# Kernel tuning notes

Hardware: AMD Instinct MI355X
Metric: run time of the kernel (lower is better)

Reference implementation:

```python
import jax, jax.numpy as jnp
import numpy as np

L_LAYERS = 6
DIM = 256
HEADS = 8
FFN = 1024
EPS_LN = 1e-3  # keras LayerNormalization default epsilon
EPS_ATT = 1e-6


def sine_pos_encoding(seq_len, d):
    pos = jnp.arange(seq_len, dtype=jnp.float32)[:, None]
    i = jnp.arange(d, dtype=jnp.float32)[None, :]
    rate = jnp.power(1e4, -(2.0 * jnp.floor(i / 2.0)) / d)
    ang = pos * rate
    return jnp.where(jnp.arange(d)[None, :] % 2 == 0, jnp.sin(ang), jnp.cos(ang))


def layer_norm(x, g, b):
    mu = jnp.mean(x, axis=-1, keepdims=True)
    var = jnp.mean(jnp.square(x - mu), axis=-1, keepdims=True)
    return (x - mu) * jax.lax.rsqrt(var + EPS_LN) * g + b


def lin_attn(xq, xk, xv, Wq, bq, Wk, bk, Wv, bv, Wo, bo):
    B, Lq, _ = xq.shape
    Lk = xk.shape[1]
    dh = DIM // HEADS
    q = (xq @ Wq + bq).reshape(B, Lq, HEADS, dh)
    k = (xk @ Wk + bk).reshape(B, Lk, HEADS, dh)
    v = (xv @ Wv + bv).reshape(B, Lk, HEADS, dh)
    # kernel feature map: elu(x) + 1
    Qf = jax.nn.elu(q) + 1.0
    Kf = jax.nn.elu(k) + 1.0
    KV = jnp.einsum('bshd,bshm->bhdm', Kf, v)            # [B,H,dh,dh]
    Z = 1.0 / (jnp.einsum('blhd,bhd->blh', Qf, Kf.sum(1)) + EPS_ATT)
    out = jnp.einsum('blhd,bhdm,blh->blhm', Qf, KV, Z)   # [B,Lq,H,dh]
    return out.reshape(B, Lq, DIM) @ Wo + bo


def setup_inputs() -> dict:
    key = jax.random.key(0)
    ks = jax.random.split(key, 32)
    s = 0.02
    d = {
        'Q': jax.random.normal(ks[0], (8, 4096, 256), jnp.float32),
        'K': jax.random.normal(ks[1], (8, 4096, 256), jnp.float32),
    }
    def W(k, shape):
        return jax.random.normal(k, shape, jnp.float32) * s
    for sfx, base in (('1', 2), ('2', 10)):
        d['Wq' + sfx] = W(ks[base + 0], (L_LAYERS, DIM, DIM))
        d['Wk' + sfx] = W(ks[base + 1], (L_LAYERS, DIM, DIM))
        d['Wv' + sfx] = W(ks[base + 2], (L_LAYERS, DIM, DIM))
        d['Wo' + sfx] = W(ks[base + 3], (L_LAYERS, DIM, DIM))
        d['bq' + sfx] = jnp.zeros((L_LAYERS, DIM))
        d['bk' + sfx] = jnp.zeros((L_LAYERS, DIM))
        d['bv' + sfx] = jnp.zeros((L_LAYERS, DIM))
        d['bo' + sfx] = jnp.zeros((L_LAYERS, DIM))
    d['Wf1'] = W(ks[20], (L_LAYERS, DIM, FFN))
    d['bf1'] = jnp.zeros((L_LAYERS, FFN))
    d['Wf2'] = W(ks[21], (L_LAYERS, FFN, DIM))
    d['bf2'] = jnp.zeros((L_LAYERS, DIM))
    for nm in ('ln1', 'ln2', 'ln3'):
        d[nm + '_g'] = jnp.ones((L_LAYERS, DIM))
        d[nm + '_b'] = jnp.zeros((L_LAYERS, DIM))
    return d


def reference(Q, K,
              Wq1, Wk1, Wv1, Wo1, bq1, bk1, bv1, bo1,
              Wq2, Wk2, Wv2, Wo2, bq2, bk2, bv2, bo2,
              Wf1, bf1, Wf2, bf2,
              ln1_g, ln1_b, ln2_g, ln2_b, ln3_g, ln3_b):
    pe = sine_pos_encoding(Q.shape[1], Q.shape[2])
    x1 = Q + pe[None]
    for i in range(L_LAYERS):
        x = lin_attn(x1, x1, x1, Wq1[i], bq1[i], Wk1[i], bk1[i], Wv1[i], bv1[i], Wo1[i], bo1[i])
        x2 = layer_norm(x + x1, ln1_g[i], ln1_b[i])
        x = lin_attn(x2, K, K, Wq2[i], bq2[i], Wk2[i], bk2[i], Wv2[i], bv2[i], Wo2[i], bo2[i])
        x3 = layer_norm(x + x2, ln2_g[i], ln2_b[i])
        h = jax.nn.relu(x3 @ Wf1[i] + bf1[i])
        f = jax.nn.relu(h @ Wf2[i] + bf2[i])  # second Dense also has relu
        x1 = layer_norm(f + x3, ln3_g[i], ln3_b[i])
    return x1
```

## Files before the change

kernel.cpp:

```cpp
#include <hip/hip_runtime.h>

#define BATCH 8
#define SEQ 4096
#define DIM 256
#define NH 8
#define DH 32
#define FFN_DIM 1024
#define NL 6
#define M_TOTAL (BATCH * SEQ)
#define NCHUNK 8

typedef __attribute__((ext_vector_type(8))) short s16x8;
typedef __attribute__((ext_vector_type(4))) short s16x4;
typedef __attribute__((ext_vector_type(4))) float f32x4;

__device__ __forceinline__ float bf2f(short s) {
    union { unsigned u; float f; } x;
    x.u = ((unsigned)(unsigned short)s) << 16;
    return x.f;
}
__device__ __forceinline__ short f2bf(float f) {
    union { float f; unsigned u; } x;
    x.f = f;
    unsigned r = x.u + 0x7fffu + ((x.u >> 16) & 1u);
    return (short)(r >> 16);
}

#define GLDS16(gp, sp) __builtin_amdgcn_global_load_lds( \
    (const __attribute__((address_space(1))) void*)(gp), \
    (__attribute__((address_space(3))) void*)(sp), 16, 0, 0)

__device__ __forceinline__ int xcd_chunk(int bx, int nwg) {
    return (bx & 7) * (nwg >> 3) + (bx >> 3);
}

__global__ void peadd_kernel(const float* __restrict__ Q, short* __restrict__ xb,
                             float* __restrict__ xf, int total)
{
    const float c = 9.210340371976184f / 256.f;
    for (int idx = blockIdx.x * 256 + threadIdx.x; idx < total; idx += gridDim.x * 256) {
        int d = idx & (DIM - 1);
        int l = (idx >> 8) & (SEQ - 1);
        float rate = __expf(-(float)(d & ~1) * c);
        float ang = (float)l * rate;
        float pe = (d & 1) ? cosf(ang) : sinf(ang);
        float v = Q[idx] + pe;
        xb[idx] = f2bf(v);
        xf[idx] = v;
    }
}

__global__ void kconv_kernel(const float* __restrict__ src, short* __restrict__ dst, int total)
{
    for (int idx = blockIdx.x * 256 + threadIdx.x; idx < total; idx += gridDim.x * 256)
        dst[idx] = f2bf(src[idx]);
}

__global__ void wtrans_kernel(const float* __restrict__ W, short* __restrict__ Wt,
                              int K, int N, int lstride, int rowoff)
{
    __shared__ float tile[32][33];
    int k0 = blockIdx.x * 32, n0 = blockIdx.y * 32;
    const float* Wl = W + (long)blockIdx.z * K * N;
    short* Wtl = Wt + (long)blockIdx.z * lstride;
    int tx = threadIdx.x, ty = threadIdx.y;
#pragma unroll
    for (int r = 0; r < 4; ++r)
        tile[ty + r * 8][tx] = Wl[(long)(k0 + ty + r * 8) * N + n0 + tx];
    __syncthreads();
#pragma unroll
    for (int r = 0; r < 4; ++r)
        Wtl[(long)(rowoff + n0 + ty + r * 8) * K + k0 + tx] = f2bf(tile[tx][ty + r * 8]);
}

__global__ void bpack_kernel(const float* __restrict__ bk1, const float* __restrict__ bv1,
                             const float* __restrict__ bk2, const float* __restrict__ bv2,
                             float* __restrict__ o1, float* __restrict__ o2)
{
    int z = blockIdx.x, t = threadIdx.x;
    o1[z * 512 + t] = (t < 256) ? bk1[z * 256 + t] : bv1[z * 256 + t - 256];
    o2[z * 512 + t] = (t < 256) ? bk2[z * 256 + t] : bv2[z * 256 + t - 256];
}

template<int ACT>
__global__ __launch_bounds__(256, 2) void gemm_bt_kernel(
    const short* __restrict__ A, const short* __restrict__ Bt,
    const float* __restrict__ bias, short* __restrict__ Cb,
    int N, int K, int lda, int ldc, int eluCut)
{
    __shared__ short As[2][128][64];
    __shared__ short Bs[2][128][64];
    const int tid = threadIdx.x;
    const int lane = tid & 63;
    const int wid = tid >> 6;
    const int wr = wid >> 1, wc = wid & 1;
    const int bx = xcd_chunk(blockIdx.x, gridDim.x);
    const int bm = bx * 128, bn = blockIdx.y * 128;
    const int l15 = lane & 15, l4 = lane >> 4;
    const int rl = lane >> 3;
    const int ch = lane & 7;
    const int nt = K >> 6;

    auto STAGE = [&](int buf, int t) {
        const int k0 = t << 6;
#pragma unroll
        for (int j = 0; j < 8; ++j) {
            int s = wid * 8 + j;
            if (s < 16) {
                int r = s * 8 + rl;
                int cs = ch ^ (r & 7);
                GLDS16(A + (long)(bm + r) * lda + k0 + cs * 8, &As[buf][s * 8][0]);
            } else {
                int r = (s - 16) * 8 + rl;
                int cs = ch ^ (r & 7);
                GLDS16(Bt + (long)(bn + r) * K + k0 + cs * 8, &Bs[buf][(s - 16) * 8][0]);
            }
        }
    };

    f32x4 acc[4][4] = {};

    STAGE(0, 0);
    STAGE(1, 1);
    for (int t = 0; t < nt; ++t) {
        const int buf = t & 1;
        if (t + 1 < nt) { asm volatile("s_waitcnt vmcnt(8)" ::: "memory"); }
        else            { asm volatile("s_waitcnt vmcnt(0)" ::: "memory"); }
        asm volatile("s_barrier" ::: "memory");
        s16x8 avA[2][4], avB[2][4];
        const int sw = l15 & 7;
#pragma unroll
        for (int kk = 0; kk < 2; ++kk) {
#pragma unroll
            for (int m = 0; m < 4; ++m)
                avA[kk][m] = *(const s16x8*)&As[buf][wr * 64 + m * 16 + l15][(((kk << 2) | l4) ^ sw) << 3];
#pragma unroll
            for (int n = 0; n < 4; ++n)
                avB[kk][n] = *(const s16x8*)&Bs[buf][wc * 64 + n * 16 + l15][(((kk << 2) | l4) ^ sw) << 3];
        }
        asm volatile("s_waitcnt lgkmcnt(0)" ::: "memory");
        asm volatile("s_barrier" ::: "memory");
        if (t + 2 < nt) STAGE(buf, t + 2);
#pragma unroll
        for (int kk = 0; kk < 2; ++kk)
#pragma unroll
            for (int m = 0; m < 4; ++m)
#pragma unroll
                for (int n = 0; n < 4; ++n)
                    acc[m][n] = __builtin_amdgcn_mfma_f32_16x16x32_bf16(avA[kk][m], avB[kk][n], acc[m][n], 0, 0, 0);
    }

#pragma unroll
    for (int m = 0; m < 4; ++m) {
        int row0 = bm + wr * 64 + m * 16 + l4 * 4;
#pragma unroll
        for (int n = 0; n < 4; ++n) {
            int col = bn + wc * 64 + n * 16 + l15;
            float bv = bias[col];
#pragma unroll
            for (int j = 0; j < 4; ++j) {
                float v = acc[m][n][j] + bv;
                if (ACT == 1) { if (col < eluCut) v = (v > 0.f) ? v + 1.f : __expf(v); }
                else if (ACT == 2) v = fmaxf(v, 0.f);
                Cb[(long)(row0 + j) * ldc + col] = f2bf(v);
            }
        }
    }
}

__global__ __launch_bounds__(512, 1) void ffnln_kernel(
    const short* __restrict__ X, const short* __restrict__ W1t,
    const float* __restrict__ b1, const short* __restrict__ W2t,
    const float* __restrict__ b2,
    const float* __restrict__ gam, const float* __restrict__ bet,
    const float* __restrict__ Fin, float* __restrict__ Fout,
    short* __restrict__ xb)
{
    __shared__ short xs[4][64][64];
    __shared__ short hs[4][64][64];
    __shared__ short Bs[8][2][32][64];
    __shared__ float partS[8][64];
    __shared__ float partQ[8][64];
    __shared__ float muA[64];
    __shared__ float rsA[64];
    const int tid = threadIdx.x;
    const int lane = tid & 63;
    const int w = tid >> 6;
    const int bm = xcd_chunk(blockIdx.x, gridDim.x) * 64;
    const int l15 = lane & 15, l4 = lane >> 4;
    const int rl = lane >> 3;
    const int ch = lane & 7;
    const int sw = l15 & 7;

#pragma unroll
    for (int j = 0; j < 4; ++j) {
        int s = w * 4 + j;
        int kt = s >> 3, rg = s & 7;
        int r = rg * 8 + rl;
        int cs = ch ^ (r & 7);
        GLDS16(X + (long)(bm + r) * 256 + kt * 64 + cs * 8, &xs[kt][rg * 8][0]);
    }
    auto STAGEB = [&](int buf, int v) {
        int hc = v >> 3, u = v & 7;
#pragma unroll
        for (int j = 0; j < 4; ++j) {
            int lr = j * 8 + rl;
            int r = w * 32 + lr;
            int cs = ch ^ (lr & 7);
            const short* src = (u < 4)
                ? W1t + (long)(hc * 256 + r) * 256 + u * 64 + cs * 8
                : W2t + (long)r * 1024 + hc * 256 + (u - 4) * 64 + cs * 8;
            GLDS16(src, &Bs[w][buf][j * 8][0]);
        }
    };

    STAGEB(0, 0);
    STAGEB(1, 1);
    asm volatile("s_waitcnt vmcnt(8)" ::: "memory");
    asm volatile("s_barrier" ::: "memory");

    f32x4 facc[4][2] = {};

    for (int hc = 0; hc < 4; ++hc) {
        f32x4 hacc[4][2] = {};
#pragma unroll
        for (int u = 0; u < 4; ++u) {
            const int v = hc * 8 + u;
            const int buf = v & 1;
            asm volatile("s_waitcnt vmcnt(4)" ::: "memory");
            s16x8 avA[2][4], avB[2][2];
#pragma unroll
            for (int kk = 0; kk < 2; ++kk) {
#pragma unroll
                for (int n = 0; n < 2; ++n)
                    avB[kk][n] = *(const s16x8*)&Bs[w][buf][n * 16 + l15][(((kk << 2) | l4) ^ sw) << 3];
#pragma unroll
                for (int m = 0; m < 4; ++m)
                    avA[kk][m] = *(const s16x8*)&xs[u][m * 16 + l15][(((kk << 2) | l4) ^ sw) << 3];
            }
            asm volatile("s_waitcnt lgkmcnt(0)" ::: "memory");
            STAGEB(buf, v + 2);
#pragma unroll
            for (int kk = 0; kk < 2; ++kk)
#pragma unroll
                for (int m = 0; m < 4; ++m)
#pragma unroll
                    for (int n = 0; n < 2; ++n)
                        hacc[m][n] = __builtin_amdgcn_mfma_f32_16x16x32_bf16(avA[kk][m], avB[kk][n], hacc[m][n], 0, 0, 0);
        }
        asm volatile("s_waitcnt lgkmcnt(0)" ::: "memory");
        asm volatile("s_barrier" ::: "memory");
#pragma unroll
        for (int m = 0; m < 4; ++m)
#pragma unroll
            for (int n = 0; n < 2; ++n) {
                int c = w * 32 + n * 16 + l15;
                float bv = b1[hc * 256 + c];
#pragma unroll
                for (int j = 0; j < 4; ++j) {
                    int r = m * 16 + l4 * 4 + j;
                    float hv = fmaxf(hacc[m][n][j] + bv, 0.f);
                    int kt = c >> 6, cc = (c & 63) >> 3;
                    hs[kt][r][((cc ^ (r & 7)) << 3) + (c & 7)] = f2bf(hv);
                }
            }
        asm volatile("s_waitcnt lgkmcnt(0)" ::: "memory");
        asm volatile("s_barrier" ::: "memory");
#pragma unroll
        for (int u = 4; u < 8; ++u) {
            const int v = hc * 8 + u;
            const int buf = v & 1;
            if (v < 31) { asm volatile("s_waitcnt vmcnt(4)" ::: "memory"); }
            else        { asm volatile("s_waitcnt vmcnt(0)" ::: "memory"); }
            s16x8 avA[2][4], avB[2][2];
#pragma unroll
            for (int kk = 0; kk < 2; ++kk) {
#pragma unroll
                for (int n = 0; n < 2; ++n)
                    avB[kk][n] = *(const s16x8*)&Bs[w][buf][n * 16 + l15][(((kk << 2) | l4) ^ sw) << 3];
#pragma unroll
                for (int m = 0; m < 4; ++m)
                    avA[kk][m] = *(const s16x8*)&hs[u - 4][m * 16 + l15][(((kk << 2) | l4) ^ sw) << 3];
            }
            asm volatile("s_waitcnt lgkmcnt(0)" ::: "memory");
            if (v + 2 < 32) STAGEB(buf, v + 2);
#pragma unroll
            for (int kk = 0; kk < 2; ++kk)
#pragma unroll
                for (int m = 0; m < 4; ++m)
#pragma unroll
                    for (int n = 0; n < 2; ++n)
                        facc[m][n] = __builtin_amdgcn_mfma_f32_16x16x32_bf16(avA[kk][m], avB[kk][n], facc[m][n], 0, 0, 0);
        }
    }

#pragma unroll
    for (int m = 0; m < 4; ++m)
#pragma unroll
        for (int n = 0; n < 2; ++n) {
            int col = w * 32 + n * 16 + l15;
            float bv = b2[col];
#pragma unroll
            for (int j = 0; j < 4; ++j) {
                int r = m * 16 + l4 * 4 + j;
                float v = fmaxf(facc[m][n][j] + bv, 0.f);
                v += Fin[(long)(bm + r) * DIM + col];
                facc[m][n][j] = v;
            }
        }
#pragma unroll
    for (int m = 0; m < 4; ++m)
#pragma unroll
        for (int j = 0; j < 4; ++j) {
            float s = facc[m][0][j] + facc[m][1][j];
            float q = facc[m][0][j] * facc[m][0][j] + facc[m][1][j] * facc[m][1][j];
#pragma unroll
            for (int off = 1; off < 16; off <<= 1) {
                s += __shfl_xor(s, off);
                q += __shfl_xor(q, off);
            }
            if (l15 == 0) {
                partS[w][m * 16 + l4 * 4 + j] = s;
                partQ[w][m * 16 + l4 * 4 + j] = q;
            }
        }
    __syncthreads();
    if (tid < 64) {
        float S = 0, Qq = 0;
#pragma unroll
        for (int ww = 0; ww < 8; ++ww) { S += partS[ww][tid]; Qq += partQ[ww][tid]; }
        float mu = S * (1.f / 256.f);
        float var = Qq * (1.f / 256.f) - mu * mu;
        muA[tid] = mu;
        rsA[tid] = rsqrtf(var + 1e-3f);
    }
    __syncthreads();
#pragma unroll
    for (int m = 0; m < 4; ++m)
#pragma unroll
        for (int j = 0; j < 4; ++j) {
            int r = m * 16 + l4 * 4 + j;
            float mu = muA[r], rs = rsA[r];
#pragma unroll
            for (int n = 0; n < 2; ++n) {
                int col = w * 32 + n * 16 + l15;
                float t = (facc[m][n][j] - mu) * rs * gam[col] + bet[col];
                long o = (long)(bm + r) * DIM + col;
                xb[o] = f2bf(t);
                Fout[o] = t;
            }
        }
}

__global__ __launch_bounds__(512, 1) void qattn_kernel(
    const short* __restrict__ A, const short* __restrict__ Bt,
    const float* __restrict__ bias, const float* __restrict__ kv,
    const float* __restrict__ ksum,
    const short* __restrict__ WoT, const float* __restrict__ bo,
    const float* __restrict__ gam, const float* __restrict__ bet,
    const float* __restrict__ Fin, float* __restrict__ Fout,
    short* __restrict__ xb)
{
    __shared__ char smem[140288];
    short (*As)[128][64] = (short(*)[128][64])(smem);
    short (*Bs)[256][64] = (short(*)[256][64])(smem + 32768);
    short (*QfL)[256] = (short(*)[256])(smem);
    short (*kvbT)[32][48] = (short(*)[32][48])(smem + 98304);
    float* ksumAll = (float*)(smem + 122880);
    float (*partDenH)[128] = (float(*)[128])(smem + 123904);
    short (*oL)[256] = (short(*)[256])(smem + 65536);
    short (*WoS)[256][64] = (short(*)[256][64])(smem);
    float (*partS)[128] = (float(*)[128])(smem + 131072);
    float (*partQ)[128] = (float(*)[128])(smem + 135168);
    float* muA = (float*)(smem + 139264);
    float* rsA = (float*)(smem + 139776);

    const int tid = threadIdx.x;
    const int lane = tid & 63;
    const int w = tid >> 6;
    const int wr = w >> 2, wc = w & 3;
    const int bm = xcd_chunk(blockIdx.x, gridDim.x) * 128;
    const int b = bm >> 12;
    const int l15 = lane & 15, l4 = lane >> 4;
    const int rl = lane >> 3;
    const int ch = lane & 7;
    const int sw = l15 & 7;

    for (int idx = tid; idx < 8192; idx += 512) {
        int h = idx >> 10, j = idx & 1023, d = j >> 5, m = j & 31;
        kvbT[h][m][d] = f2bf(kv[(long)(b * 8 + h) * 1024 + j]);
    }
    if (tid < 256) ksumAll[tid] = ksum[(b * 8 + (tid >> 5)) * 32 + (tid & 31)];

    auto STAGE = [&](int buf, int t) {
        const int k0 = t << 6;
#pragma unroll
        for (int j = 0; j < 6; ++j) {
            int s = w * 6 + j;
            if (s < 16) {
                int r = s * 8 + rl;
                int cs = ch ^ (r & 7);
                GLDS16(A + (long)(bm + r) * 256 + k0 + cs * 8, &As[buf][s * 8][0]);
            } else {
                int r = (s - 16) * 8 + rl;
                int cs = ch ^ (r & 7);
                GLDS16(Bt + (long)r * 256 + k0 + cs * 8, &Bs[buf][(s - 16) * 8][0]);
            }
        }
    };

    f32x4 acc[4][4] = {};

    STAGE(0, 0);
    STAGE(1, 1);
#pragma unroll
    for (int t = 0; t < 4; ++t) {
        const int buf = t & 1;
        if (t < 3) { asm volatile("s_waitcnt vmcnt(6)" ::: "memory"); }
        else       { asm volatile("s_waitcnt vmcnt(0)" ::: "memory"); }
        asm volatile("s_barrier" ::: "memory");
        s16x8 avA[2][4], avB[2][4];
#pragma unroll
        for (int kk = 0; kk < 2; ++kk) {
#pragma unroll
            for (int m = 0; m < 4; ++m)
                avA[kk][m] = *(const s16x8*)&As[buf][wr * 64 + m * 16 + l15][(((kk << 2) | l4) ^ sw) << 3];
#pragma unroll
            for (int n = 0; n < 4; ++n)
                avB[kk][n] = *(const s16x8*)&Bs[buf][wc * 64 + n * 16 + l15][(((kk << 2) | l4) ^ sw) << 3];
        }
        asm volatile("s_waitcnt lgkmcnt(0)" ::: "memory");
        asm volatile("s_barrier" ::: "memory");
        if (t < 2) STAGE(buf, t + 2);
#pragma unroll
        for (int kk = 0; kk < 2; ++kk)
#pragma unroll
            for (int m = 0; m < 4; ++m)
#pragma unroll
                for (int n = 0; n < 4; ++n)
                    acc[m][n] = __builtin_amdgcn_mfma_f32_16x16x32_bf16(avA[kk][m], avB[kk][n], acc[m][n], 0, 0, 0);
    }

#pragma unroll
    for (int m = 0; m < 4; ++m)
#pragma unroll
        for (int n = 0; n < 4; ++n) {
            int col = wc * 64 + n * 16 + l15;
            float bv = bias[col];
#pragma unroll
            for (int j = 0; j < 4; ++j) {
                float v = acc[m][n][j] + bv;
                acc[m][n][j] = (v > 0.f) ? v + 1.f : __expf(v);
            }
        }
#pragma unroll
    for (int m = 0; m < 4; ++m)
#pragma unroll
        for (int j = 0; j < 4; ++j) {
            float p0 = acc[m][0][j] * ksumAll[wc * 64 + l15]
                     + acc[m][1][j] * ksumAll[wc * 64 + 16 + l15];
            float p1 = acc[m][2][j] * ksumAll[wc * 64 + 32 + l15]
                     + acc[m][3][j] * ksumAll[wc * 64 + 48 + l15];
#pragma unroll
            for (int off = 1; off < 16; off <<= 1) {
                p0 += __shfl_xor(p0, off);
                p1 += __shfl_xor(p1, off);
            }
            if (l15 == 0) {
                int r = wr * 64 + m * 16 + l4 * 4 + j;
                partDenH[wc * 2 + 0][r] = p0;
                partDenH[wc * 2 + 1][r] = p1;
            }
        }
#pragma unroll
    for (int m = 0; m < 4; ++m)
#pragma unroll
        for (int n = 0; n < 4; ++n) {
            int col = wc * 64 + n * 16 + l15;
#pragma unroll
            for (int j = 0; j < 4; ++j) {
                int r = wr * 64 + m * 16 + l4 * 4 + j;
                int chunk = (col >> 3) ^ (r & 7);
                QfL[r][chunk * 8 + (col & 7)] = f2bf(acc[m][n][j]);
            }
        }
    __syncthreads();

    const int h = w;
    s16x8 afr[2];
#pragma unroll
    for (int ct = 0; ct < 2; ++ct)
        afr[ct] = *(const s16x8*)&kvbT[h][ct * 16 + l15][l4 * 8];
    float zv[8];
#pragma unroll
    for (int rt = 0; rt < 8; ++rt)
        zv[rt] = 1.f / (partDenH[h][rt * 16 + l15] + 1e-6f);
    asm volatile("s_waitcnt lgkmcnt(0)" ::: "memory");
    __syncthreads();

#pragma unroll
    for (int rt = 0; rt < 8; ++rt) {
        int r = rt * 16 + l15;
        int qchunk = (h * 4 + l4) ^ (r & 7);
        s16x8 bfr = *(const s16x8*)&QfL[r][qchunk * 8];
#pragma unroll
        for (int ct = 0; ct < 2; ++ct) {
            f32x4 zero = {0.f, 0.f, 0.f, 0.f};
            f32x4 po = __builtin_amdgcn_mfma_f32_16x16x32_bf16(afr[ct], bfr, zero, 0, 0, 0);
            s16x4 o4;
#pragma unroll
            for (int j = 0; j < 4; ++j) o4[j] = f2bf(po[j] * zv[rt]);
            int c0 = h * 32 + ct * 16 + l4 * 4;
            int cc = c0 >> 3;
            *(s16x4*)&oL[r][((cc ^ (r & 7)) << 3) + (c0 & 7)] = o4;
        }
    }
    asm volatile("s_waitcnt lgkmcnt(0)" ::: "memory");
    __syncthreads();

    auto STAGEWO = [&](int buf, int t) {
#pragma unroll
        for (int j = 0; j < 4; ++j) {
            int lr = j * 8 + rl;
            int r = w * 32 + lr;
            int cs = ch ^ (lr & 7);
            GLDS16(WoT + (long)r * 256 + t * 64 + cs * 8, &WoS[buf][w * 32 + j * 8][0]);
        }
    };
    STAGEWO(0, 0);
    STAGEWO(1, 1);

    f32x4 facc[8][2] = {};
#pragma unroll
    for (int t = 0; t < 4; ++t) {
        const int buf = t & 1;
        if (t < 3) { asm volatile("s_waitcnt vmcnt(4)" ::: "memory"); }
        else       { asm volatile("s_waitcnt vmcnt(0)" ::: "memory"); }
#pragma unroll
        for (int kk = 0; kk < 2; ++kk) {
            s16x8 avB0 = *(const s16x8*)&WoS[buf][w * 32 + l15][(((kk << 2) | l4) ^ sw) << 3];
            s16x8 avB1 = *(const s16x8*)&WoS[buf][w * 32 + 16 + l15][(((kk << 2) | l4) ^ sw) << 3];
#pragma unroll
            for (int m = 0; m < 8; ++m) {
                int ar = m * 16 + l15;
                s16x8 avA = *(const s16x8*)&oL[ar][(t * 8 + (((kk << 2) | l4) ^ sw)) << 3];
                facc[m][0] = __builtin_amdgcn_mfma_f32_16x16x32_bf16(avA, avB0, facc[m][0], 0, 0, 0);
                facc[m][1] = __builtin_amdgcn_mfma_f32_16x16x32_bf16(avA, avB1, facc[m][1], 0, 0, 0);
            }
        }
        asm volatile("s_waitcnt lgkmcnt(0)" ::: "memory");
        if (t + 2 < 4) STAGEWO(buf, t + 2);
    }

#pragma unroll
    for (int m = 0; m < 8; ++m)
#pragma unroll
        for (int n = 0; n < 2; ++n) {
            int col = w * 32 + n * 16 + l15;
            float bv = bo[col];
#pragma unroll
            for (int j = 0; j < 4; ++j) {
                int r = m * 16 + l4 * 4 + j;
                float v = facc[m][n][j] + bv;
                v += Fin[(long)(bm + r) * DIM + col];
                facc[m][n][j] = v;
            }
        }
#pragma unroll
    for (int m = 0; m < 8; ++m)
#pragma unroll
        for (int j = 0; j < 4; ++j) {
            float s = facc[m][0][j] + facc[m][1][j];
            float q = facc[m][0][j] * facc[m][0][j] + facc[m][1][j] * facc[m][1][j];
#pragma unroll
            for (int off = 1; off < 16; off <<= 1) {
                s += __shfl_xor(s, off);
                q += __shfl_xor(q, off);
            }
            if (l15 == 0) {
                partS[w][m * 16 + l4 * 4 + j] = s;
                partQ[w][m * 16 + l4 * 4 + j] = q;
            }
        }
    __syncthreads();
    if (tid < 128) {
        float S = 0, Qq = 0;
#pragma unroll
        for (int ww = 0; ww < 8; ++ww) { S += partS[ww][tid]; Qq += partQ[ww][tid]; }
        float mu = S * (1.f / 256.f);
        float var = Qq * (1.f / 256.f) - mu * mu;
        muA[tid] = mu;
        rsA[tid] = rsqrtf(var + 1e-3f);
    }
    __syncthreads();
#pragma unroll
    for (int m = 0; m < 8; ++m)
#pragma unroll
        for (int j = 0; j < 4; ++j) {
            int r = m * 16 + l4 * 4 + j;
            float mu = muA[r], rs = rsA[r];
#pragma unroll
            for (int n = 0; n < 2; ++n) {
                int col = w * 32 + n * 16 + l15;
                float t = (facc[m][n][j] - mu) * rs * gam[col] + bet[col];
                long o = (long)(bm + r) * DIM + col;
                xb[o] = f2bf(t);
                Fout[o] = t;
            }
        }
}

__global__ __launch_bounds__(256) void kvpart_kernel(
    const short* __restrict__ KV, float* __restrict__ part)
{
    __shared__ float kfs[32][32];
    __shared__ float vsh[32][32];
    int flat = blockIdx.x + (blockIdx.y << 3);
    int b = flat & 7;
    int hh = (flat >> 3) & 7, c = flat >> 6;
    int bh = b * 8 + hh;
    int tid = threadIdx.x;
    int d = tid >> 3, m0 = (tid & 7) * 4;
    float acc0 = 0, acc1 = 0, acc2 = 0, acc3 = 0, ks = 0;
    long rowBase = ((long)b * SEQ + c * 512) * 512 + hh * DH;
    int lrow = (tid & 127) >> 2, cg = tid & 3;
    for (int s0 = 0; s0 < 512; s0 += 32) {
        long rb = rowBase + (long)(s0 + lrow) * 512 + cg * 8 + ((tid < 128) ? 0 : 256);
        s16x8 v8 = *(const s16x8*)(KV + rb);
        float* dst = (tid < 128) ? &kfs[lrow][cg * 8] : &vsh[lrow][cg * 8];
#pragma unroll
        for (int e = 0; e < 8; ++e) dst[e] = bf2f(v8[e]);
        __syncthreads();
#pragma unroll
        for (int s = 0; s < 32; ++s) {
            float kd = kfs[s][d];
            acc0 += kd * vsh[s][m0];
            acc1 += kd * vsh[s][m0 + 1];
            acc2 += kd * vsh[s][m0 + 2];
            acc3 += kd * vsh[s][m0 + 3];
        }
        if (tid < 32) {
#pragma unroll
            for (int s = 0; s < 32; ++s) ks += kfs[s][tid];
        }
        __syncthreads();
    }
    float* pb = part + ((long)bh * NCHUNK + c) * 1056;
    pb[tid * 4 + 0] = acc0; pb[tid * 4 + 1] = acc1;
    pb[tid * 4 + 2] = acc2; pb[tid * 4 + 3] = acc3;
    if (tid < 32) pb[1024 + tid] = ks;
}

__global__ __launch_bounds__(256) void kvred_kernel(
    const float* __restrict__ part, float* __restrict__ kv, float* __restrict__ ksum)
{
    int bh = blockIdx.x, tid = threadIdx.x;
    const float* pb = part + (long)bh * NCHUNK * 1056;
    float s0 = 0, s1 = 0, s2 = 0, s3 = 0;
    for (int cc = 0; cc < NCHUNK; ++cc) {
        const float* p = pb + cc * 1056 + tid * 4;
        s0 += p[0]; s1 += p[1]; s2 += p[2]; s3 += p[3];
    }
    float* kb = kv + (long)bh * 1024 + tid * 4;
    kb[0] = s0; kb[1] = s1; kb[2] = s2; kb[3] = s3;
    if (tid < 32) {
        float ss = 0;
        for (int cc = 0; cc < NCHUNK; ++cc) ss += pb[cc * 1056 + 1024 + tid];
        ksum[bh * 32 + tid] = ss;
    }
}

extern "C" void kernel_launch(void* const* d_in, const int* in_sizes, int n_in,
                              void* d_out, int out_size, void* d_ws, size_t ws_size,
                              hipStream_t stream)
{
    const float* Qin = (const float*)d_in[0];
    const float* Kin = (const float*)d_in[1];
    const float* Wq1 = (const float*)d_in[2];
    const float* Wk1 = (const float*)d_in[3];
    const float* Wv1 = (const float*)d_in[4];
    const float* Wo1 = (const float*)d_in[5];
    const float* bq1 = (const float*)d_in[6];
    const float* bk1 = (const float*)d_in[7];
    const float* bv1 = (const float*)d_in[8];
    const float* bo1 = (const float*)d_in[9];
    const float* Wq2 = (const float*)d_in[10];
    const float* Wk2 = (const float*)d_in[11];
    const float* Wv2 = (const float*)d_in[12];
    const float* Wo2 = (const float*)d_in[13];
    const float* bq2 = (const float*)d_in[14];
    const float* bk2 = (const float*)d_in[15];
    const float* bv2 = (const float*)d_in[16];
    const float* bo2 = (const float*)d_in[17];
    const float* Wf1 = (const float*)d_in[18];
    const float* bf1 = (const float*)d_in[19];
    const float* Wf2 = (const float*)d_in[20];
    const float* bf2 = (const float*)d_in[21];
    const float* ln1g = (const float*)d_in[22];
    const float* ln1b = (const float*)d_in[23];
    const float* ln2g = (const float*)d_in[24];
    const float* ln2b = (const float*)d_in[25];
    const float* ln3g = (const float*)d_in[26];
    const float* ln3b = (const float*)d_in[27];
    (void)in_sizes; (void)n_in; (void)out_size;

    const size_t NEED = 117841920ULL;
    if (ws_size < NEED) return;

    char* ws = (char*)d_ws;
    size_t off = 0;
    auto alloc = [&](size_t bytes) -> void* {
        void* p = ws + off;
        off = (off + bytes + 255) & ~(size_t)255;
        return p;
    };
    const size_t ACT_E = (size_t)M_TOTAL * DIM;

    short* wkv1t = (short*)alloc((size_t)NL * 512 * 256 * 2);
    short* wkv2t = (short*)alloc((size_t)NL * 512 * 256 * 2);
    short* wq1t  = (short*)alloc((size_t)NL * 65536 * 2);
    short* wo1t  = (short*)alloc((size_t)NL * 65536 * 2);
    short* wq2t  = (short*)alloc((size_t)NL * 65536 * 2);
    short* wo2t  = (short*)alloc((size_t)NL * 65536 * 2);
    short* wf1t  = (short*)alloc((size_t)NL * 262144 * 2);
    short* wf2t  = (short*)alloc((size_t)NL * 262144 * 2);
    float* bkv1  = (float*)alloc((size_t)NL * 512 * 4);
    float* bkv2  = (float*)alloc((size_t)NL * 512 * 4);
    short* kbf = (short*)alloc(ACT_E * 2);
    short* A0  = (short*)alloc(ACT_E * 2);
    short* BIG = (short*)alloc((size_t)M_TOTAL * 512 * 2);
    float* Fx  = (float*)alloc(ACT_E * 4);
    float* part = (float*)alloc((size_t)64 * NCHUNK * 1056 * 4);
    float* kvb  = (float*)alloc((size_t)64 * 1024 * 4);
    float* ksb  = (float*)alloc((size_t)64 * 32 * 4);

    peadd_kernel<<<2048, 256, 0, stream>>>(Qin, A0, Fx, (int)ACT_E);
    kconv_kernel<<<2048, 256, 0, stream>>>(Kin, kbf, (int)ACT_E);
    wtrans_kernel<<<dim3(8, 8, NL), dim3(32, 8), 0, stream>>>(Wk1, wkv1t, 256, 256, 512 * 256, 0);
    wtrans_kernel<<<dim3(8, 8, NL), dim3(32, 8), 0, stream>>>(Wv1, wkv1t, 256, 256, 512 * 256, 256);
    wtrans_kernel<<<dim3(8, 8, NL), dim3(32, 8), 0, stream>>>(Wk2, wkv2t, 256, 256, 512 * 256, 0);
    wtrans_kernel<<<dim3(8, 8, NL), dim3(32, 8), 0, stream>>>(Wv2, wkv2t, 256, 256, 512 * 256, 256);
    wtrans_kernel<<<dim3(8, 8, NL), dim3(32, 8), 0, stream>>>(Wq1, wq1t, 256, 256, 65536, 0);
    wtrans_kernel<<<dim3(8, 8, NL), dim3(32, 8), 0, stream>>>(Wo1, wo1t, 256, 256, 65536, 0);
    wtrans_kernel<<<dim3(8, 8, NL), dim3(32, 8), 0, stream>>>(Wq2, wq2t, 256, 256, 65536, 0);
    wtrans_kernel<<<dim3(8, 8, NL), dim3(32, 8), 0, stream>>>(Wo2, wo2t, 256, 256, 65536, 0);
    wtrans_kernel<<<dim3(8, 32, NL), dim3(32, 8), 0, stream>>>(Wf1, wf1t, 256, 1024, 262144, 0);
    wtrans_kernel<<<dim3(32, 8, NL), dim3(32, 8), 0, stream>>>(Wf2, wf2t, 1024, 256, 262144, 0);
    bpack_kernel<<<NL, 512, 0, stream>>>(bk1, bv1, bk2, bv2, bkv1, bkv2);

    dim3 blk(256), blk512(512);

    for (int i = 0; i < NL; ++i) {
        const short* wkv1i = wkv1t + (size_t)i * 512 * 256;
        const short* wkv2i = wkv2t + (size_t)i * 512 * 256;
        const short* wq1i = wq1t + (size_t)i * 65536;
        const short* wo1i = wo1t + (size_t)i * 65536;
        const short* wq2i = wq2t + (size_t)i * 65536;
        const short* wo2i = wo2t + (size_t)i * 65536;
        const short* wf1i = wf1t + (size_t)i * 262144;
        const short* wf2i = wf2t + (size_t)i * 262144;

        gemm_bt_kernel<1><<<dim3(256, 4), blk, 0, stream>>>(A0, wkv1i, bkv1 + i * 512, BIG, 512, 256, 256, 512, 256);
        kvpart_kernel<<<dim3(NCHUNK, 64), blk, 0, stream>>>(BIG, part);
        kvred_kernel<<<64, blk, 0, stream>>>(part, kvb, ksb);
        qattn_kernel<<<M_TOTAL / 128, blk512, 0, stream>>>(A0, wq1i, bq1 + i * 256, kvb, ksb,
            wo1i, bo1 + i * 256, ln1g + i * 256, ln1b + i * 256, Fx, Fx, A0);

        gemm_bt_kernel<1><<<dim3(256, 4), blk, 0, stream>>>(kbf, wkv2i, bkv2 + i * 512, BIG, 512, 256, 256, 512, 256);
        kvpart_kernel<<<dim3(NCHUNK, 64), blk, 0, stream>>>(BIG, part);
        kvred_kernel<<<64, blk, 0, stream>>>(part, kvb, ksb);
        qattn_kernel<<<M_TOTAL / 128, blk512, 0, stream>>>(A0, wq2i, bq2 + i * 256, kvb, ksb,
            wo2i, bo2 + i * 256, ln2g + i * 256, ln2b + i * 256, Fx, Fx, A0);

        ffnln_kernel<<<M_TOTAL / 64, blk512, 0, stream>>>(A0, wf1i, bf1 + i * 1024,
            wf2i, bf2 + i * 256, ln3g + i * 256, ln3b + i * 256,
            Fx, (i == NL - 1) ? (float*)d_out : Fx, A0);
    }
}
```

Before: 1.359 ms.

## Fuse K/V projection with per-chunk KV outer-product reduction using MFMA

The K/V projection GEMM now stages its 128-row, two-head output tile (Kf after elu+1, and V) transposed in shared memory. It then computes the per-chunk Kf^T·V partial and the Kf column sums directly with MFMA, so the bf16 K/V intermediate no longer makes a round trip through global memory. The separate scalar FP32 kvpart kernel and the BIG buffer are removed. In exchange, NCHUNK rises to 32, so kvred sums four times more partials, and the Kf/V values are rounded to bf16 before the MFMA reduction.

Measured after the change: 1.124 ms, median of 2. 1.21x faster.

```diff
diff --git a/kernel.cpp b/kernel.cpp
--- a/kernel.cpp
+++ b/kernel.cpp
@@ -8,7 +8,7 @@
 #define FFN_DIM 1024
 #define NL 6
 #define M_TOTAL (BATCH * SEQ)
-#define NCHUNK 8
+#define NCHUNK 32
 
 typedef __attribute__((ext_vector_type(8))) short s16x8;
 typedef __attribute__((ext_vector_type(4))) short s16x4;
@@ -82,11 +82,9 @@
     o2[z * 512 + t] = (t < 256) ? bk2[z * 256 + t] : bv2[z * 256 + t - 256];
 }
 
-template<int ACT>
-__global__ __launch_bounds__(256, 2) void gemm_bt_kernel(
-    const short* __restrict__ A, const short* __restrict__ Bt,
-    const float* __restrict__ bias, short* __restrict__ Cb,
-    int N, int K, int lda, int ldc, int eluCut)
+__global__ __launch_bounds__(256, 2) void kvproj_kernel(
+    const short* __restrict__ A, const short* __restrict__ WkvT,
+    const float* __restrict__ bkv, float* __restrict__ part)
 {
     __shared__ short As[2][128][64];
     __shared__ short Bs[2][128][64];
@@ -94,12 +92,14 @@
     const int lane = tid & 63;
     const int wid = tid >> 6;
     const int wr = wid >> 1, wc = wid & 1;
+    const int p = blockIdx.y;
     const int bx = xcd_chunk(blockIdx.x, gridDim.x);
-    const int bm = bx * 128, bn = blockIdx.y * 128;
+    const int bm = bx * 128;
+    const int b = bx >> 5, chunk = bx & 31;
     const int l15 = lane & 15, l4 = lane >> 4;
     const int rl = lane >> 3;
     const int ch = lane & 7;
-    const int nt = K >> 6;
+    const int sw = l15 & 7;
 
     auto STAGE = [&](int buf, int t) {
         const int k0 = t << 6;
@@ -109,11 +109,12 @@
             if (s < 16) {
                 int r = s * 8 + rl;
                 int cs = ch ^ (r & 7);
-                GLDS16(A + (long)(bm + r) * lda + k0 + cs * 8, &As[buf][s * 8][0]);
+                GLDS16(A + (long)(bm + r) * 256 + k0 + cs * 8, &As[buf][s * 8][0]);
             } else {
                 int r = (s - 16) * 8 + rl;
+                int srcRow = (r < 64) ? (p * 64 + r) : (256 + p * 64 + (r - 64));
                 int cs = ch ^ (r & 7);
-                GLDS16(Bt + (long)(bn + r) * K + k0 + cs * 8, &Bs[buf][(s - 16) * 8][0]);
+                GLDS16(WkvT + (long)srcRow * 256 + k0 + cs * 8, &Bs[buf][(s - 16) * 8][0]);
             }
         }
     };
@@ -122,13 +123,12 @@
 
     STAGE(0, 0);
     STAGE(1, 1);
-    for (int t = 0; t < nt; ++t) {
+    for (int t = 0; t < 4; ++t) {
         const int buf = t & 1;
-        if (t + 1 < nt) { asm volatile("s_waitcnt vmcnt(8)" ::: "memory"); }
-        else            { asm volatile("s_waitcnt vmcnt(0)" ::: "memory"); }
+        if (t < 3) { asm volatile("s_waitcnt vmcnt(8)" ::: "memory"); }
+        else       { asm volatile("s_waitcnt vmcnt(0)" ::: "memory"); }
         asm volatile("s_barrier" ::: "memory");
         s16x8 avA[2][4], avB[2][4];
-        const int sw = l15 & 7;
 #pragma unroll
         for (int kk = 0; kk < 2; ++kk) {
 #pragma unroll
@@ -140,7 +140,7 @@
         }
         asm volatile("s_waitcnt lgkmcnt(0)" ::: "memory");
         asm volatile("s_barrier" ::: "memory");
-        if (t + 2 < nt) STAGE(buf, t + 2);
+        if (t + 2 < 4) STAGE(buf, t + 2);
 #pragma unroll
         for (int kk = 0; kk < 2; ++kk)
 #pragma unroll
@@ -149,22 +149,80 @@
                 for (int n = 0; n < 4; ++n)
                     acc[m][n] = __builtin_amdgcn_mfma_f32_16x16x32_bf16(avA[kk][m], avB[kk][n], acc[m][n], 0, 0, 0);
     }
-
-#pragma unroll
-    for (int m = 0; m < 4; ++m) {
-        int row0 = bm + wr * 64 + m * 16 + l4 * 4;
+    short (*KfT)[136] = (short(*)[136])&As[0][0][0];
+    short (*VfT)[136] = (short(*)[136])&Bs[0][0][0];
+
+#pragma unroll
+    for (int m = 0; m < 4; ++m)
 #pragma unroll
         for (int n = 0; n < 4; ++n) {
-            int col = bn + wc * 64 + n * 16 + l15;
-            float bv = bias[col];
+            int c = wc * 64 + n * 16 + l15;
+            float bv = (c < 64) ? bkv[p * 64 + c] : bkv[256 + p * 64 + (c - 64)];
 #pragma unroll
             for (int j = 0; j < 4; ++j) {
+                int r = wr * 64 + m * 16 + l4 * 4 + j;
                 float v = acc[m][n][j] + bv;
-                if (ACT == 1) { if (col < eluCut) v = (v > 0.f) ? v + 1.f : __expf(v); }
-                else if (ACT == 2) v = fmaxf(v, 0.f);
-                Cb[(long)(row0 + j) * ldc + col] = f2bf(v);
-            }
-        }
+                if (c < 64) {
+                    v = (v > 0.f) ? v + 1.f : __expf(v);
+                    KfT[c][r] = f2bf(v);
+                } else {
+                    VfT[c - 64][r] = f2bf(v);
+                }
+            }
+        }
+    __syncthreads();
+
+    const int hl = wid & 1, dt = wid >> 1;
+    f32x4 acc2[2] = {{0.f, 0.f, 0.f, 0.f}, {0.f, 0.f, 0.f, 0.f}};
+#pragma unroll
+    for (int kc = 0; kc < 4; ++kc) {
+        s16x8 af = *(const s16x8*)&KfT[hl * 32 + dt * 16 + l15][kc * 32 + l4 * 8];
+#pragma unroll
+        for (int mt = 0; mt < 2; ++mt) {
+            s16x8 bf = *(const s16x8*)&VfT[hl * 32 + mt * 16 + l15][kc * 32 + l4 * 8];
+            acc2[mt] = __builtin_amdgcn_mfma_f32_16x16x32_bf16(af, bf, acc2[mt], 0, 0, 0);
+        }
+    }
+    const int h = 2 * p + hl;
+    float* pb = part + ((long)(b * 8 + h) * NCHUNK + chunk) * 1056;
+#pragma unroll
+    for (int mt = 0; mt < 2; ++mt)
+#pragma unroll
+        for (int j = 0; j < 4; ++j) {
+            int d = dt * 16 + l4 * 4 + j;
+            int mm = mt * 16 + l15;
+            pb[d * 32 + mm] = acc2[mt][j];
+        }
+    if (tid < 64) {
+        float s = 0.f;
+#pragma unroll
+        for (int rr = 0; rr < 16; ++rr) {
+            s16x8 v8 = *(const s16x8*)&KfT[tid][rr * 8];
+#pragma unroll
+            for (int e = 0; e < 8; ++e) s += bf2f(v8[e]);
+        }
+        int hh = tid >> 5, dd = tid & 31;
+        float* pb2 = part + ((long)(b * 8 + 2 * p + hh) * NCHUNK + chunk) * 1056;
+        pb2[1024 + dd] = s;
+    }
+}
+
+__global__ __launch_bounds__(256) void kvred_kernel(
+    const float* __restrict__ part, float* __restrict__ kv, float* __restrict__ ksum)
+{
+    int bh = blockIdx.x, tid = threadIdx.x;
+    const float* pb = part + (long)bh * NCHUNK * 1056;
+    float s0 = 0, s1 = 0, s2 = 0, s3 = 0;
+    for (int cc = 0; cc < NCHUNK; ++cc) {
+        const float* ptr = pb + cc * 1056 + tid * 4;
+        s0 += ptr[0]; s1 += ptr[1]; s2 += ptr[2]; s3 += ptr[3];
+    }
+    float* kb = kv + (long)bh * 1024 + tid * 4;
+    kb[0] = s0; kb[1] = s1; kb[2] = s2; kb[3] = s3;
+    if (tid < 32) {
+        float ss = 0;
+        for (int cc = 0; cc < NCHUNK; ++cc) ss += pb[cc * 1056 + 1024 + tid];
+        ksum[bh * 32 + tid] = ss;
     }
 }
 
@@ -608,66 +666,6 @@
                 Fout[o] = t;
             }
         }
-}
-
-__global__ __launch_bounds__(256) void kvpart_kernel(
-    const short* __restrict__ KV, float* __restrict__ part)
-{
-    __shared__ float kfs[32][32];
-    __shared__ float vsh[32][32];
-    int flat = blockIdx.x + (blockIdx.y << 3);
-    int b = flat & 7;
-    int hh = (flat >> 3) & 7, c = flat >> 6;
-    int bh = b * 8 + hh;
-    int tid = threadIdx.x;
-    int d = tid >> 3, m0 = (tid & 7) * 4;
-    float acc0 = 0, acc1 = 0, acc2 = 0, acc3 = 0, ks = 0;
-    long rowBase = ((long)b * SEQ + c * 512) * 512 + hh * DH;
-    int lrow = (tid & 127) >> 2, cg = tid & 3;
-    for (int s0 = 0; s0 < 512; s0 += 32) {
-        long rb = rowBase + (long)(s0 + lrow) * 512 + cg * 8 + ((tid < 128) ? 0 : 256);
-        s16x8 v8 = *(const s16x8*)(KV + rb);
-        float* dst = (tid < 128) ? &kfs[lrow][cg * 8] : &vsh[lrow][cg * 8];
-#pragma unroll
-        for (int e = 0; e < 8; ++e) dst[e] = bf2f(v8[e]);
-        __syncthreads();
-#pragma unroll
-        for (int s = 0; s < 32; ++s) {
-            float kd = kfs[s][d];
-            acc0 += kd * vsh[s][m0];
-            acc1 += kd * vsh[s][m0 + 1];
-            acc2 += kd * vsh[s][m0 + 2];
-            acc3 += kd * vsh[s][m0 + 3];
-        }
-        if (tid < 32) {
-#pragma unroll
-            for (int s = 0; s < 32; ++s) ks += kfs[s][tid];
-        }
-        __syncthreads();
-    }
-    float* pb = part + ((long)bh * NCHUNK + c) * 1056;
-    pb[tid * 4 + 0] = acc0; pb[tid * 4 + 1] = acc1;
-    pb[tid * 4 + 2] = acc2; pb[tid * 4 + 3] = acc3;
-    if (tid < 32) pb[1024 + tid] = ks;
-}
-
-__global__ __launch_bounds__(256) void kvred_kernel(
-    const float* __restrict__ part, float* __restrict__ kv, float* __restrict__ ksum)
-{
-    int bh = blockIdx.x, tid = threadIdx.x;
-    const float* pb = part + (long)bh * NCHUNK * 1056;
-    float s0 = 0, s1 = 0, s2 = 0, s3 = 0;
-    for (int cc = 0; cc < NCHUNK; ++cc) {
-        const float* p = pb + cc * 1056 + tid * 4;
-        s0 += p[0]; s1 += p[1]; s2 += p[2]; s3 += p[3];
-    }
-    float* kb = kv + (long)bh * 1024 + tid * 4;
-    kb[0] = s0; kb[1] = s1; kb[2] = s2; kb[3] = s3;
-    if (tid < 32) {
-        float ss = 0;
-        for (int cc = 0; cc < NCHUNK; ++cc) ss += pb[cc * 1056 + 1024 + tid];
-        ksum[bh * 32 + tid] = ss;
-    }
 }
 
 extern "C" void kernel_launch(void* const* d_in, const int* in_sizes, int n_in,
@@ -728,7 +726,6 @@
     float* bkv2  = (float*)alloc((size_t)NL * 512 * 4);
     short* kbf = (short*)alloc(ACT_E * 2);
     short* A0  = (short*)alloc(ACT_E * 2);
-    short* BIG = (short*)alloc((size_t)M_TOTAL * 512 * 2);
     float* Fx  = (float*)alloc(ACT_E * 4);
     float* part = (float*)alloc((size_t)64 * NCHUNK * 1056 * 4);
     float* kvb  = (float*)alloc((size_t)64 * 1024 * 4);
@@ -760,14 +757,12 @@
         const short* wf1i = wf1t + (size_t)i * 262144;
         const short* wf2i = wf2t + (size_t)i * 262144;
 
-        gemm_bt_kernel<1><<<dim3(256, 4), blk, 0, stream>>>(A0, wkv1i, bkv1 + i * 512, BIG, 512, 256, 256, 512, 256);
-        kvpart_kernel<<<dim3(NCHUNK, 64), blk, 0, stream>>>(BIG, part);
+        kvproj_kernel<<<dim3(256, 4), blk, 0, stream>>>(A0, wkv1i, bkv1 + i * 512, part);
         kvred_kernel<<<64, blk, 0, stream>>>(part, kvb, ksb);
         qattn_kernel<<<M_TOTAL / 128, blk512, 0, stream>>>(A0, wq1i, bq1 + i * 256, kvb, ksb,
             wo1i, bo1 + i * 256, ln1g + i * 256, ln1b + i * 256, Fx, Fx, A0);
 
-        gemm_bt_kernel<1><<<dim3(256, 4), blk, 0, stream>>>(kbf, wkv2i, bkv2 + i * 512, BIG, 512, 256, 256, 512, 256);
-        kvpart_kernel<<<dim3(NCHUNK, 64), blk, 0, stream>>>(BIG, part);
+        kvproj_kernel<<<dim3(256, 4), blk, 0, stream>>>(kbf, wkv2i, bkv2 + i * 512, part);
         kvred_kernel<<<64, blk, 0, stream>>>(part, kvb, ksb);
         qattn_kernel<<<M_TOTAL / 128, blk512, 0, stream>>>(A0, wq2i, bq2 + i * 256, kvb, ksb,
             wo2i, bo2 + i * 256, ln2g + i * 256, ln2b + i * 256, Fx, Fx, A0);
```
